# Performance work log

Measured on AMD Instinct MI355X. Metric: run time of the kernel, lower is better.

Reference implementation:

```python
import jax, jax.numpy as jnp
import numpy as np

B, N, D = 32, 2048, 128
SQRT_DIM = np.sqrt(float(D)).astype(np.float32)  # scale=True -> 1/sqrt(dim)
MASK_FILL = -65504.0  # value used by masked_fill_ in the torch module


def setup_inputs() -> dict:
    key = jax.random.key(0)
    kq, kk, kv = jax.random.split(key, 3)
    return {
        "query": jax.random.normal(kq, (B, N, D), dtype=jnp.float32),
        "key": jax.random.normal(kk, (B, N, D), dtype=jnp.float32),
        "value": jax.random.normal(kv, (B, N, D), dtype=jnp.float32),
        "mask": jnp.ones((B, N, N), dtype=bool),
    }


def reference(query, key, value, mask):
    # score = Q K^T / sqrt(d)   -> [B, N, N]
    score = jnp.einsum("bnd,bmd->bnm", query, key) / SQRT_DIM
    # masked_fill_(~mask, -65504)
    score = jnp.where(mask, score, MASK_FILL)
    attn = jax.nn.softmax(score, axis=-1)
    # context = attn @ V        -> [B, N, D]
    context = jnp.einsum("bnm,bmd->bnd", attn, value)
    return (context, attn)
```

## Files before the change

### kernel.cpp

```cpp
#include <hip/hip_runtime.h>
#include <stdint.h>

#define B_ 32
#define N_ 2048
#define D_ 128
#define TQ 16
#define NW 8
#define CPW (N_ / NW)
#define NT (CPW / 16)
#define SCALE 0.08838834764831845f
#define MASK_FILL -65504.0f

typedef __attribute__((ext_vector_type(8))) short short8;
typedef __attribute__((ext_vector_type(4))) float f32x4;
typedef __attribute__((ext_vector_type(4))) int i32x4;
typedef __attribute__((ext_vector_type(4))) unsigned short ushort4_t;
typedef unsigned short ushort_t;

static __device__ __forceinline__ short f2bf(float f) {
    unsigned u = __builtin_bit_cast(unsigned, f);
    u += 0x7FFFu + ((u >> 16) & 1u);
    return (short)(u >> 16);
}

__global__ __launch_bounds__(256)
void conv_bf16_kernel(const float* __restrict__ X, ushort_t* __restrict__ Y) {
    const size_t i = ((size_t)blockIdx.x * 256 + threadIdx.x) * 8;
    f32x4 a = *(const f32x4*)(X + i);
    f32x4 c = *(const f32x4*)(X + i + 4);
    short8 o;
    #pragma unroll
    for (int j = 0; j < 4; ++j) { o[j] = f2bf(a[j]); o[4 + j] = f2bf(c[j]); }
    *(short8*)(Y + i) = o;
}

__global__ __launch_bounds__(256)
void conv_vt_kernel(const float* __restrict__ V, ushort_t* __restrict__ Vt) {
    __shared__ ushort_t t[32][34];
    const int tid = threadIdx.x;
    const int b = blockIdx.z, n0 = blockIdx.x * 32, d0 = blockIdx.y * 32;
    {
        const int r = tid >> 3, cg = (tid & 7) * 4;
        f32x4 v = *(const f32x4*)(V + ((size_t)b * N_ + n0 + r) * D_ + d0 + cg);
        #pragma unroll
        for (int j = 0; j < 4; ++j) t[r][cg + j] = (ushort_t)f2bf(v[j]);
    }
    __syncthreads();
    {
        const int d = tid >> 3, ng = (tid & 7) * 4;
        ushort4_t o = { t[ng][d], t[ng + 1][d], t[ng + 2][d], t[ng + 3][d] };
        *(ushort4_t*)(Vt + ((size_t)b * D_ + d0 + d) * N_ + n0 + ng) = o;
    }
}

template <int PRE>
__global__ __launch_bounds__(512, 4)
void attn_fused_kernel(const float* __restrict__ Q, const float* __restrict__ K,
                       const ushort_t* __restrict__ Kb, const float* __restrict__ V,
                       const ushort_t* __restrict__ Vt, const int* __restrict__ mask,
                       float* __restrict__ attn, float* __restrict__ ctx) {
    extern __shared__ char smem[];
    char*  Pb   = smem;
    float* redm = (float*)(smem + TQ * N_ * 2);
    float* reds = redm + NW * TQ;

    int wg = blockIdx.x;
    wg = (wg & 7) * (4096 / 8) + (wg >> 3);
    const int b    = wg >> 7;
    const int row0 = (wg & 127) * TQ;

    const int tid  = threadIdx.x;
    const int w    = tid >> 6;
    const int lane = tid & 63;
    const int l16  = lane & 15;
    const int quad = lane >> 4;

    const size_t qkvbase = (size_t)b * N_ * D_;

    short8 qf[4];
    {
        const float* qp = Q + qkvbase + (size_t)(row0 + l16) * D_ + quad * 8;
        #pragma unroll
        for (int kt = 0; kt < 4; ++kt) {
            f32x4 x = *(const f32x4*)(qp + kt * 32);
            f32x4 y = *(const f32x4*)(qp + kt * 32 + 4);
            #pragma unroll
            for (int j = 0; j < 4; ++j) { qf[kt][j] = f2bf(x[j]); qf[kt][4 + j] = f2bf(y[j]); }
        }
    }

    const int* mrow = mask + ((size_t)b * N_ + row0 + l16) * N_ + w * CPW + quad * 4;
    f32x4 acc[NT];
    float mmax = -INFINITY;
    #pragma unroll
    for (int t = 0; t < NT; ++t) {
        const int c0 = w * CPW + t * 16;
        i32x4 mv = __builtin_nontemporal_load((const i32x4*)(mrow + t * 16));
        f32x4 a = {0.f, 0.f, 0.f, 0.f};
        if constexpr (PRE) {
            const ushort_t* kp = Kb + qkvbase + (size_t)(c0 + l16) * D_ + quad * 8;
            #pragma unroll
            for (int kt = 0; kt < 4; ++kt) {
                short8 kf = *(const short8*)(kp + kt * 32);
                a = __builtin_amdgcn_mfma_f32_16x16x32_bf16(kf, qf[kt], a, 0, 0, 0);
            }
        } else {
            const float* kp = K + qkvbase + (size_t)(c0 + l16) * D_ + quad * 8;
            #pragma unroll
            for (int kt = 0; kt < 4; ++kt) {
                f32x4 x = *(const f32x4*)(kp + kt * 32);
                f32x4 y = *(const f32x4*)(kp + kt * 32 + 4);
                short8 kf;
                #pragma unroll
                for (int j = 0; j < 4; ++j) { kf[j] = f2bf(x[j]); kf[4 + j] = f2bf(y[j]); }
                a = __builtin_amdgcn_mfma_f32_16x16x32_bf16(kf, qf[kt], a, 0, 0, 0);
            }
        }
        #pragma unroll
        for (int r = 0; r < 4; ++r) {
            float s = mv[r] ? a[r] * SCALE : MASK_FILL;
            a[r] = s;
            mmax = fmaxf(mmax, s);
        }
        acc[t] = a;
    }

    mmax = fmaxf(mmax, __shfl_xor(mmax, 16));
    mmax = fmaxf(mmax, __shfl_xor(mmax, 32));
    if (quad == 0) redm[w * TQ + l16] = mmax;
    __syncthreads();
    float m = redm[l16];
    #pragma unroll
    for (int w2 = 1; w2 < NW; ++w2) m = fmaxf(m, redm[w2 * TQ + l16]);

    float sum = 0.f;
    #pragma unroll
    for (int t = 0; t < NT; ++t) {
        #pragma unroll
        for (int r = 0; r < 4; ++r) {
            float e = __expf(acc[t][r] - m);
            acc[t][r] = e;
            sum += e;
        }
    }
    sum += __shfl_xor(sum, 16);
    sum += __shfl_xor(sum, 32);
    if (quad == 0) reds[w * TQ + l16] = sum;
    __syncthreads();
    float rsum = reds[l16];
    #pragma unroll
    for (int w2 = 1; w2 < NW; ++w2) rsum += reds[w2 * TQ + l16];
    const float inv = 1.f / rsum;

    float* arow = attn + ((size_t)b * N_ + row0 + l16) * N_ + w * CPW + quad * 4;
    const unsigned pbase = (unsigned)(l16 * (N_ * 2) + (w * CPW + quad * 4) * 2);
    const unsigned swz   = (unsigned)((l16 & 7) << 4);
    #pragma unroll
    for (int t = 0; t < NT; ++t) {
        f32x4 vout;
        #pragma unroll
        for (int r = 0; r < 4; ++r) vout[r] = acc[t][r] * inv;
        __builtin_nontemporal_store(vout, (f32x4*)(arow + t * 16));
        unsigned lo = (unsigned)(unsigned short)f2bf(vout[0]) | ((unsigned)(unsigned short)f2bf(vout[1]) << 16);
        unsigned hi = (unsigned)(unsigned short)f2bf(vout[2]) | ((unsigned)(unsigned short)f2bf(vout[3]) << 16);
        *(unsigned long long*)(Pb + ((pbase + t * 32) ^ swz)) = ((unsigned long long)hi << 32) | lo;
    }
    __syncthreads();

    const int n0 = w * 16;
    f32x4 o0 = {0.f, 0.f, 0.f, 0.f};
    f32x4 o1 = {0.f, 0.f, 0.f, 0.f};
    const unsigned prbase = (unsigned)(l16 * (N_ * 2) + quad * 16);
    if constexpr (PRE) {
        const ushort_t* vrow = Vt + qkvbase + (size_t)(n0 + l16) * N_ + quad * 8;
        #pragma unroll 2
        for (int kk = 0; kk < N_; kk += 64) {
            short8 pf0 = *(const short8*)(Pb + ((prbase + kk * 2) ^ swz));
            short8 pf1 = *(const short8*)(Pb + ((prbase + kk * 2 + 64) ^ swz));
            short8 vf0 = *(const short8*)(vrow + kk);
            short8 vf1 = *(const short8*)(vrow + kk + 32);
            o0 = __builtin_amdgcn_mfma_f32_16x16x32_bf16(vf0, pf0, o0, 0, 0, 0);
            o1 = __builtin_amdgcn_mfma_f32_16x16x32_bf16(vf1, pf1, o1, 0, 0, 0);
        }
    } else {
        const float* vcol = V + qkvbase + (size_t)(quad * 8) * D_ + n0 + l16;
        #pragma unroll 2
        for (int kk = 0; kk < N_; kk += 64) {
            short8 pf0 = *(const short8*)(Pb + ((prbase + kk * 2) ^ swz));
            short8 pf1 = *(const short8*)(Pb + ((prbase + kk * 2 + 64) ^ swz));
            short8 vf0, vf1;
            #pragma unroll
            for (int j = 0; j < 8; ++j) {
                vf0[j] = f2bf(vcol[(size_t)(kk + j) * D_]);
                vf1[j] = f2bf(vcol[(size_t)(kk + 32 + j) * D_]);
            }
            o0 = __builtin_amdgcn_mfma_f32_16x16x32_bf16(vf0, pf0, o0, 0, 0, 0);
            o1 = __builtin_amdgcn_mfma_f32_16x16x32_bf16(vf1, pf1, o1, 0, 0, 0);
        }
    }
    f32x4 o = o0 + o1;
    float* crow = ctx + ((size_t)b * N_ + row0 + l16) * D_ + n0 + quad * 4;
    __builtin_nontemporal_store(o, (f32x4*)crow);
}

extern "C" void kernel_launch(void* const* d_in, const int* in_sizes, int n_in,
                              void* d_out, int out_size, void* d_ws, size_t ws_size,
                              hipStream_t stream) {
    const float* Q    = (const float*)d_in[0];
    const float* K    = (const float*)d_in[1];
    const float* V    = (const float*)d_in[2];
    const int*   mask = (const int*)d_in[3];

    float* out  = (float*)d_out;
    float* ctx  = out;
    float* attn = out + (size_t)B_ * N_ * D_;

    dim3 grid(B_ * (N_ / TQ), 1, 1);
    dim3 block(512, 1, 1);
    const size_t lds = (size_t)TQ * N_ * 2 + 2 * NW * TQ * sizeof(float);

    const size_t nel = (size_t)B_ * N_ * D_;
    const size_t ws_need = nel * 2 * 2;

    if (ws_size >= ws_need) {
        ushort_t* Kb = (ushort_t*)d_ws;
        ushort_t* Vt = Kb + nel;
        conv_bf16_kernel<<<dim3((unsigned)(nel / 8 / 256)), dim3(256), 0, stream>>>(K, Kb);
        conv_vt_kernel<<<dim3(N_ / 32, D_ / 32, B_), dim3(256), 0, stream>>>(V, Vt);
        attn_fused_kernel<1><<<grid, block, lds, stream>>>(Q, K, Kb, V, Vt, mask, attn, ctx);
    } else {
        attn_fused_kernel<0><<<grid, block, lds, stream>>>(Q, K, (const ushort_t*)nullptr,
                                                           V, (const ushort_t*)nullptr,
                                                           mask, attn, ctx);
    }
}
```

Before: 1.415 ms.

## Software-pipeline K, mask and V loads with register double-buffering in attention kernel

In the pre-converted bf16 path, the QK^T loop now prefetches K fragments two tiles ahead and mask vectors four tiles ahead into rotating register buffers. The PV loop is fully unrolled and prefetches V two steps and P one step ahead, spreading work over four accumulators to break MFMA dependency chains. Nontemporal loads and stores for mask, attn and ctx become ordinary ones. The aim is to hide global-memory latency behind MFMA work, at the cost of higher register pressure and possibly lower occupancy.

```diff
diff --git a/kernel.cpp b/kernel.cpp
--- a/kernel.cpp
+++ b/kernel.cpp
@@ -92,20 +92,52 @@
     const int* mrow = mask + ((size_t)b * N_ + row0 + l16) * N_ + w * CPW + quad * 4;
     f32x4 acc[NT];
     float mmax = -INFINITY;
-    #pragma unroll
-    for (int t = 0; t < NT; ++t) {
-        const int c0 = w * CPW + t * 16;
-        i32x4 mv = __builtin_nontemporal_load((const i32x4*)(mrow + t * 16));
-        f32x4 a = {0.f, 0.f, 0.f, 0.f};
-        if constexpr (PRE) {
-            const ushort_t* kp = Kb + qkvbase + (size_t)(c0 + l16) * D_ + quad * 8;
-            #pragma unroll
-            for (int kt = 0; kt < 4; ++kt) {
-                short8 kf = *(const short8*)(kp + kt * 32);
-                a = __builtin_amdgcn_mfma_f32_16x16x32_bf16(kf, qf[kt], a, 0, 0, 0);
-            }
-        } else {
+
+    if constexpr (PRE) {
+        const ushort_t* kbase = Kb + qkvbase + (size_t)(w * CPW + l16) * D_ + quad * 8;
+        short8 kfb[2][4];
+        i32x4  mvb[4];
+        #pragma unroll
+        for (int p = 0; p < 2; ++p) {
+            const ushort_t* kp = kbase + (size_t)(p * 16) * D_;
+            #pragma unroll
+            for (int kt = 0; kt < 4; ++kt) kfb[p][kt] = *(const short8*)(kp + kt * 32);
+        }
+        #pragma unroll
+        for (int p = 0; p < 4; ++p) mvb[p] = *(const i32x4*)(mrow + p * 16);
+
+        #pragma unroll
+        for (int t = 0; t < NT; ++t) {
+            short8 kf0 = kfb[t & 1][0], kf1 = kfb[t & 1][1];
+            short8 kf2 = kfb[t & 1][2], kf3 = kfb[t & 1][3];
+            i32x4  mv  = mvb[t & 3];
+            if (t + 2 < NT) {
+                const ushort_t* kp = kbase + (size_t)((t + 2) * 16) * D_;
+                #pragma unroll
+                for (int kt = 0; kt < 4; ++kt) kfb[t & 1][kt] = *(const short8*)(kp + kt * 32);
+            }
+            if (t + 4 < NT) mvb[t & 3] = *(const i32x4*)(mrow + (t + 4) * 16);
+
+            f32x4 a = {0.f, 0.f, 0.f, 0.f};
+            a = __builtin_amdgcn_mfma_f32_16x16x32_bf16(kf0, qf[0], a, 0, 0, 0);
+            a = __builtin_amdgcn_mfma_f32_16x16x32_bf16(kf1, qf[1], a, 0, 0, 0);
+            a = __builtin_amdgcn_mfma_f32_16x16x32_bf16(kf2, qf[2], a, 0, 0, 0);
+            a = __builtin_amdgcn_mfma_f32_16x16x32_bf16(kf3, qf[3], a, 0, 0, 0);
+            #pragma unroll
+            for (int r = 0; r < 4; ++r) {
+                float s = mv[r] ? a[r] * SCALE : MASK_FILL;
+                a[r] = s;
+                mmax = fmaxf(mmax, s);
+            }
+            acc[t] = a;
+        }
+    } else {
+        #pragma unroll
+        for (int t = 0; t < NT; ++t) {
+            const int c0 = w * CPW + t * 16;
+            i32x4 mv = *(const i32x4*)(mrow + t * 16);
             const float* kp = K + qkvbase + (size_t)(c0 + l16) * D_ + quad * 8;
+            f32x4 a = {0.f, 0.f, 0.f, 0.f};
             #pragma unroll
             for (int kt = 0; kt < 4; ++kt) {
                 f32x4 x = *(const f32x4*)(kp + kt * 32);
@@ -115,14 +147,14 @@
                 for (int j = 0; j < 4; ++j) { kf[j] = f2bf(x[j]); kf[4 + j] = f2bf(y[j]); }
                 a = __builtin_amdgcn_mfma_f32_16x16x32_bf16(kf, qf[kt], a, 0, 0, 0);
             }
-        }
-        #pragma unroll
-        for (int r = 0; r < 4; ++r) {
-            float s = mv[r] ? a[r] * SCALE : MASK_FILL;
-            a[r] = s;
-            mmax = fmaxf(mmax, s);
-        }
-        acc[t] = a;
+            #pragma unroll
+            for (int r = 0; r < 4; ++r) {
+                float s = mv[r] ? a[r] * SCALE : MASK_FILL;
+                a[r] = s;
+                mmax = fmaxf(mmax, s);
+            }
+            acc[t] = a;
+        }
     }
 
     mmax = fmaxf(mmax, __shfl_xor(mmax, 16));
@@ -160,7 +192,7 @@
         f32x4 vout;
         #pragma unroll
         for (int r = 0; r < 4; ++r) vout[r] = acc[t][r] * inv;
-        __builtin_nontemporal_store(vout, (f32x4*)(arow + t * 16));
+        *(f32x4*)(arow + t * 16) = vout;
         unsigned lo = (unsigned)(unsigned short)f2bf(vout[0]) | ((unsigned)(unsigned short)f2bf(vout[1]) << 16);
         unsigned hi = (unsigned)(unsigned short)f2bf(vout[2]) | ((unsigned)(unsigned short)f2bf(vout[3]) << 16);
         *(unsigned long long*)(Pb + ((pbase + t * 32) ^ swz)) = ((unsigned long long)hi << 32) | lo;
@@ -168,19 +200,39 @@
     __syncthreads();
 
     const int n0 = w * 16;
-    f32x4 o0 = {0.f, 0.f, 0.f, 0.f};
-    f32x4 o1 = {0.f, 0.f, 0.f, 0.f};
+    f32x4 o0 = {0.f, 0.f, 0.f, 0.f}, o1 = {0.f, 0.f, 0.f, 0.f};
+    f32x4 o2 = {0.f, 0.f, 0.f, 0.f}, o3 = {0.f, 0.f, 0.f, 0.f};
     const unsigned prbase = (unsigned)(l16 * (N_ * 2) + quad * 16);
     if constexpr (PRE) {
         const ushort_t* vrow = Vt + qkvbase + (size_t)(n0 + l16) * N_ + quad * 8;
-        #pragma unroll 2
-        for (int kk = 0; kk < N_; kk += 64) {
-            short8 pf0 = *(const short8*)(Pb + ((prbase + kk * 2) ^ swz));
-            short8 pf1 = *(const short8*)(Pb + ((prbase + kk * 2 + 64) ^ swz));
-            short8 vf0 = *(const short8*)(vrow + kk);
-            short8 vf1 = *(const short8*)(vrow + kk + 32);
-            o0 = __builtin_amdgcn_mfma_f32_16x16x32_bf16(vf0, pf0, o0, 0, 0, 0);
-            o1 = __builtin_amdgcn_mfma_f32_16x16x32_bf16(vf1, pf1, o1, 0, 0, 0);
+        short8 vfb[2][2];
+        short8 pfc0, pfc1;
+        #pragma unroll
+        for (int p = 0; p < 2; ++p) {
+            vfb[p][0] = *(const short8*)(vrow + p * 64);
+            vfb[p][1] = *(const short8*)(vrow + p * 64 + 32);
+        }
+        pfc0 = *(const short8*)(Pb + ((prbase + 0) ^ swz));
+        pfc1 = *(const short8*)(Pb + ((prbase + 64) ^ swz));
+        #pragma unroll
+        for (int i = 0; i < 32; ++i) {
+            short8 v0 = vfb[i & 1][0], v1 = vfb[i & 1][1];
+            short8 p0 = pfc0, p1 = pfc1;
+            if (i + 2 < 32) {
+                vfb[i & 1][0] = *(const short8*)(vrow + (i + 2) * 64);
+                vfb[i & 1][1] = *(const short8*)(vrow + (i + 2) * 64 + 32);
+            }
+            if (i + 1 < 32) {
+                pfc0 = *(const short8*)(Pb + ((prbase + (i + 1) * 128) ^ swz));
+                pfc1 = *(const short8*)(Pb + ((prbase + (i + 1) * 128 + 64) ^ swz));
+            }
+            if (i & 1) {
+                o2 = __builtin_amdgcn_mfma_f32_16x16x32_bf16(v0, p0, o2, 0, 0, 0);
+                o3 = __builtin_amdgcn_mfma_f32_16x16x32_bf16(v1, p1, o3, 0, 0, 0);
+            } else {
+                o0 = __builtin_amdgcn_mfma_f32_16x16x32_bf16(v0, p0, o0, 0, 0, 0);
+                o1 = __builtin_amdgcn_mfma_f32_16x16x32_bf16(v1, p1, o1, 0, 0, 0);
+            }
         }
     } else {
         const float* vcol = V + qkvbase + (size_t)(quad * 8) * D_ + n0 + l16;
@@ -198,9 +250,9 @@
             o1 = __builtin_amdgcn_mfma_f32_16x16x32_bf16(vf1, pf1, o1, 0, 0, 0);
         }
     }
-    f32x4 o = o0 + o1;
+    f32x4 o = (o0 + o2) + (o1 + o3);
     float* crow = ctx + ((size_t)b * N_ + row0 + l16) * D_ + n0 + quad * 4;
-    __builtin_nontemporal_store(o, (f32x4*)crow);
+    *(f32x4*)crow = o;
 }
 
 extern "C" void kernel_launch(void* const* d_in, const int* in_sizes, int n_in,
```

Measured after the change: 1.406 ms. No clear change (-0.7%).
